# Kernel optimization log

Hardware: AMD Instinct MI355X
Metric: run time of the kernel (lower is better)

Reference implementation:

```python
import jax, jax.numpy as jnp
import numpy as np

N, M, E, H = 4096, 16384, 512, 8
D = E // H  # head dim = 64


def _rms(x, g, eps=1e-6):
    return x * jax.lax.rsqrt(jnp.mean(jnp.square(x), axis=-1, keepdims=True) + eps) * g


def _split(x):
    # (rows, E) -> (rows, H, D)
    return x.reshape(x.shape[0], H, D)


def _sdpa(q, k, v):
    # Faithful to the source layout: SDPA on (rows, H, D) tensors, i.e. per-row
    # attention over the H heads (tiny HxH softmax per node).
    s = jnp.einsum('nhd,ngd->nhg', q, k) / jnp.sqrt(jnp.asarray(D, q.dtype))
    a = jax.nn.softmax(s, axis=-1)
    return jnp.einsum('nhg,ngd->nhd', a, v).reshape(-1, E)


def setup_inputs() -> dict:
    key = jax.random.key(0)
    ks = jax.random.split(key, 25)
    w = lambda k, s, sc: jax.random.normal(k, s, dtype=jnp.float32) * sc
    se = 1.0 / np.sqrt(E)   # Linear(E, E) init scale
    sm = 1.0 / np.sqrt(M)   # Linear(M, N) init scale
    inp = {
        'x_node': jax.random.normal(ks[0], (N, E), dtype=jnp.float32),
        'x_edge': jax.random.normal(ks[1], (M, E), dtype=jnp.float32),
        # sparse-ish binary adjacency, avg degree ~8
        'adj': (jax.random.uniform(ks[2], (N, N)) < 0.002).astype(jnp.float32),
        # per-branch QKV weights (4 separate MultiHeadAttention modules)
        'Wq_hh': w(ks[3], (E, E), se), 'Wk_hh': w(ks[4], (E, E), se), 'Wv_hh': w(ks[5], (E, E), se),
        'Wq_ee': w(ks[6], (E, E), se), 'Wk_ee': w(ks[7], (E, E), se), 'Wv_ee': w(ks[8], (E, E), se),
        'Wq_he': w(ks[9], (E, E), se), 'Wk_he': w(ks[10], (E, E), se), 'Wv_he': w(ks[11], (E, E), se),
        'Wq_eh': w(ks[12], (E, E), se), 'Wk_eh': w(ks[13], (E, E), se), 'Wv_eh': w(ks[14], (E, E), se),
        # shape_proj (edges -> nodes) weights, one per module that uses it
        'Wp1_he': w(ks[15], (N, M), sm),
        'Wp1_eh': w(ks[16], (N, M), sm),
        'Wp1_ee': w(ks[17], (N, M), sm),
        # RMSNorm gains
        'g_n': jnp.ones((E,), jnp.float32),
        'g_e': jnp.ones((E,), jnp.float32),
        'g2': jnp.ones((E,), jnp.float32),
        # FeedForward
        'Wf1': w(ks[18], (E, 4 * E), se), 'bf1': jnp.zeros((4 * E,), jnp.float32),
        'Wf2': w(ks[19], (4 * E, E), 1.0 / np.sqrt(4 * E)), 'bf2': jnp.zeros((E,), jnp.float32),
    }
    return inp


def reference(x_node, x_edge, adj,
              Wq_hh, Wk_hh, Wv_hh, Wq_ee, Wk_ee, Wv_ee,
              Wq_he, Wk_he, Wv_he, Wq_eh, Wk_eh, Wv_eh,
              Wp1_he, Wp1_eh, Wp1_ee,
              g_n, g_e, g2, Wf1, bf1, Wf2, bf2):
    h = _rms(x_node, g_n)   # (N, E)
    e = _rms(x_edge, g_e)   # (M, E)

    # hh: adjacency injected into the node query branch
    q = jnp.einsum('nm,mhd->nhd', adj, _split(h @ Wq_hh))
    out_hh = _sdpa(q, _split(h @ Wk_hh), _split(h @ Wv_hh))

    # ee: edge queries/keys projected to node rows via shape_proj
    q = jnp.einsum('nm,mhd->nhd', Wp1_ee, _split(e @ Wq_ee))
    k = jnp.einsum('nm,mhd->nhd', Wp1_ee, _split(e @ Wk_ee))
    out_ee = _sdpa(q, k, _split(h @ Wv_ee))

    # eh: edge query projected to node rows, node key
    q = jnp.einsum('nm,mhd->nhd', Wp1_eh, _split(e @ Wq_eh))
    out_eh = _sdpa(q, _split(h @ Wk_eh), _split(h @ Wv_eh))

    # he: node query, edge key projected to node rows
    k = jnp.einsum('nm,mhd->nhd', Wp1_he, _split(e @ Wk_he))
    out_he = _sdpa(_split(h @ Wq_he), k, _split(h @ Wv_he))

    x = out_hh + out_ee + out_eh + out_he          # (N, E)
    y = _rms(x, g2)
    return jax.nn.gelu(y @ Wf1 + bf1, approximate=False) @ Wf2 + bf2
```

## Files before the change

### kernel.cpp

```cpp
#include <hip/hip_runtime.h>
#include <cstdint>


typedef unsigned short u16;
typedef __bf16 bf16x8 __attribute__((ext_vector_type(8)));
typedef float f32x4 __attribute__((ext_vector_type(4)));

__device__ __forceinline__ u16 f2bf(float f) {
    unsigned u = __float_as_uint(f);
    return (u16)((u + 0x7fffu + ((u >> 16) & 1u)) >> 16);
}
__device__ __forceinline__ float bf2f(u16 u) { return __uint_as_float(((unsigned)u) << 16); }
__device__ __forceinline__ float gelu_exact(float x) {
    return 0.5f * x * (1.0f + erff(x * 0.70710678118654752f));
}

__device__ __forceinline__ void gload_lds16(const void* g, void* l) {
    __builtin_amdgcn_global_load_lds(
        (const __attribute__((address_space(1))) unsigned int*)(uintptr_t)g,
        (__attribute__((address_space(3))) unsigned int*)(unsigned int)(uintptr_t)l,
        16, 0, 0);
}

__device__ __forceinline__ void swz_block(int& bx, int& by, int& bz) {
    const int nx = gridDim.x, ny = gridDim.y;
    const int nwg = nx * ny * gridDim.z;
    int lin = blockIdx.x + nx * (blockIdx.y + ny * blockIdx.z);
    const int chunk = nwg >> 3;
    lin = (lin & 7) * chunk + (lin >> 3);
    bx = lin % nx;
    lin /= nx;
    by = lin % ny;
    bz = lin / ny;
}

template <bool SWZ>
__global__ __launch_bounds__(256) void cvt_f32_bf16(const float* __restrict__ in,
                                                    u16* __restrict__ out, size_t n8) {
    size_t i = (size_t)blockIdx.x * 256 + threadIdx.x;
    size_t stride = (size_t)gridDim.x * 256;
    for (; i < n8; i += stride) {
        float4 a = ((const float4*)in)[i * 2];
        float4 b = ((const float4*)in)[i * 2 + 1];
        u16 r[8] = {f2bf(a.x), f2bf(a.y), f2bf(a.z), f2bf(a.w),
                    f2bf(b.x), f2bf(b.y), f2bf(b.z), f2bf(b.w)};
        size_t o = i;
        if constexpr (SWZ) o = (i & ~(size_t)63) | ((i & 63) ^ ((i >> 7) & 3));
        ((uint4*)out)[o] = *(const uint4*)r;
    }
}

__global__ __launch_bounds__(256) void transpose_cvt(const float* __restrict__ in,
                                                     u16* __restrict__ out, int R, int C) {
    __shared__ float tile[32][33];
    int c0 = blockIdx.x * 32, r0 = blockIdx.y * 32;
    int tx = threadIdx.x & 31, ty = threadIdx.x >> 5;
#pragma unroll
    for (int i = 0; i < 4; ++i)
        tile[ty + i * 8][tx] = in[(size_t)(r0 + ty + i * 8) * C + c0 + tx];
    __syncthreads();
#pragma unroll
    for (int i = 0; i < 4; ++i) {
        int orow = c0 + ty + i * 8;
        out[(size_t)orow * R + ((r0 + tx) ^ (((orow >> 1) & 3) << 3))] = f2bf(tile[tx][ty + i * 8]);
    }
}

struct W12 { const float* in[12]; u16* out[12]; };
__global__ __launch_bounds__(256) void transpose_cvt12(W12 w) {
    __shared__ float tile[32][33];
    const float* in = w.in[blockIdx.z];
    u16* out = w.out[blockIdx.z];
    int c0 = blockIdx.x * 32, r0 = blockIdx.y * 32;
    int tx = threadIdx.x & 31, ty = threadIdx.x >> 5;
#pragma unroll
    for (int i = 0; i < 4; ++i)
        tile[ty + i * 8][tx] = in[(size_t)(r0 + ty + i * 8) * 512 + c0 + tx];
    __syncthreads();
#pragma unroll
    for (int i = 0; i < 4; ++i) {
        int orow = c0 + ty + i * 8;
        out[(size_t)orow * 512 + ((r0 + tx) ^ (((orow >> 1) & 3) << 3))] = f2bf(tile[tx][ty + i * 8]);
    }
}

__global__ __launch_bounds__(256) void transpose_u16(const u16* __restrict__ in,
                                                     u16* __restrict__ out, int R, int C) {
    __shared__ u16 tile[32][34];
    int c0 = blockIdx.x * 32, r0 = blockIdx.y * 32;
    int tx = threadIdx.x & 31, ty = threadIdx.x >> 5;
#pragma unroll
    for (int i = 0; i < 4; ++i)
        tile[ty + i * 8][tx] = in[(size_t)(r0 + ty + i * 8) * C + c0 + tx];
    __syncthreads();
#pragma unroll
    for (int i = 0; i < 4; ++i) {
        int orow = c0 + ty + i * 8;
        out[(size_t)orow * R + ((r0 + tx) ^ (((orow >> 1) & 3) << 3))] = tile[tx][ty + i * 8];
    }
}

template <bool SWZ>
__global__ __launch_bounds__(256) void rmsnorm_bf16(const float* __restrict__ x,
                                                    const float* __restrict__ g,
                                                    u16* __restrict__ out) {
    int row = blockIdx.x, tid = threadIdx.x;
    const float* xr = x + (size_t)row * 512;
    float2 v = *(const float2*)(xr + tid * 2);
    float ss = v.x * v.x + v.y * v.y;
#pragma unroll
    for (int o = 32; o; o >>= 1) ss += __shfl_down(ss, o);
    __shared__ float red[4];
    if ((tid & 63) == 0) red[tid >> 6] = ss;
    __syncthreads();
    float tot = red[0] + red[1] + red[2] + red[3];
    float rs = rsqrtf(tot * (1.0f / 512.0f) + 1e-6f);
    unsigned pack = (unsigned)f2bf(v.x * rs * g[tid * 2]) |
                    ((unsigned)f2bf(v.y * rs * g[tid * 2 + 1]) << 16);
    int o32 = SWZ ? (tid ^ (((row >> 1) & 3) << 2)) : tid;
    ((unsigned*)out)[(size_t)row * 256 + o32] = pack;
}

__global__ __launch_bounds__(256) void adj_spmm(const float* __restrict__ adj,
                                                const u16* __restrict__ h,
                                                u16* __restrict__ out) {
    const int wave = threadIdx.x >> 6, lane = threadIdx.x & 63;
    const int n = blockIdx.x * 4 + wave;
    const float* arow = adj + (size_t)n * 4096;
    float acc[8] = {0.f, 0.f, 0.f, 0.f, 0.f, 0.f, 0.f, 0.f};
    for (int j = 0; j < 64; ++j) {
        float v = arow[j * 64 + lane];
        unsigned long long mask = __ballot(v != 0.0f);
        while (mask) {
            int bit = __ffsll((long long)mask) - 1;
            mask &= mask - 1;
            int m = j * 64 + bit;
            float w = __shfl(v, bit);
            int cs = (lane & ~3) | ((lane & 3) ^ ((m >> 1) & 3));
            uint4 q = *(const uint4*)(h + (size_t)m * 512 + cs * 8);
            const u16* qu = (const u16*)&q;
#pragma unroll
            for (int t = 0; t < 8; ++t) acc[t] += w * bf2f(qu[t]);
        }
    }
    int co = (lane & ~3) | ((lane & 3) ^ ((n >> 1) & 3));
    u16 r[8];
#pragma unroll
    for (int t = 0; t < 8; ++t) r[t] = f2bf(acc[t]);
    *(uint4*)(out + (size_t)n * 512 + co * 8) = *(const uint4*)r;
}

template <int MODE>
__device__ __forceinline__ void gemm_tile_body(const u16* __restrict__ A,
                                               const u16* __restrict__ Bt,
                                               int N, int K, int k_begin, int k_end,
                                               int rowStart, int colStart,
                                               void* __restrict__ C,
                                               const float* __restrict__ bias) {
    __shared__ u16 Asm[128 * 32];
    __shared__ u16 Bsm[128 * 32];
    const int tid = threadIdx.x;
    const int wave = tid >> 6, lane = tid & 63;
    const int wr = wave >> 1, wc = wave & 1;

    f32x4 acc[4][4];
#pragma unroll
    for (int m = 0; m < 4; ++m)
#pragma unroll
        for (int n = 0; n < 4; ++n) acc[m][n] = f32x4{0.f, 0.f, 0.f, 0.f};

    const int off0 = (wave * 2 + 0) * 1024 + lane * 16;
    const int off1 = (wave * 2 + 1) * 1024 + lane * 16;
    const int r0 = off0 >> 6, k0e = (off0 & 63) >> 1;
    const int r1 = off1 >> 6, k1e = (off1 & 63) >> 1;
    const size_t Arow0 = (size_t)(rowStart + r0) * K + k0e;
    const size_t Arow1 = (size_t)(rowStart + r1) * K + k1e;
    const size_t Brow0 = (size_t)(colStart + r0) * K + k0e;
    const size_t Brow1 = (size_t)(colStart + r1) * K + k1e;
    u16* As0 = &Asm[(wave * 2 + 0) * 512];
    u16* As1 = &Asm[(wave * 2 + 1) * 512];
    u16* Bs0 = &Bsm[(wave * 2 + 0) * 512];
    u16* Bs1 = &Bsm[(wave * 2 + 1) * 512];

    const int rsel = lane & 15, ksel = lane >> 4;
    const int fsw = (ksel ^ ((rsel >> 1) & 3)) << 3;

    for (int kk = k_begin; kk < k_end; kk += 32) {
        gload_lds16(A + Arow0 + kk, As0);
        gload_lds16(A + Arow1 + kk, As1);
        gload_lds16(Bt + Brow0 + kk, Bs0);
        gload_lds16(Bt + Brow1 + kk, Bs1);
        __syncthreads();
        bf16x8 aF[4], bF[4];
#pragma unroll
        for (int m = 0; m < 4; ++m)
            aF[m] = *(const bf16x8*)&Asm[(wr * 64 + m * 16 + rsel) * 32 + fsw];
#pragma unroll
        for (int n = 0; n < 4; ++n)
            bF[n] = *(const bf16x8*)&Bsm[(wc * 64 + n * 16 + rsel) * 32 + fsw];
#pragma unroll
        for (int m = 0; m < 4; ++m)
#pragma unroll
            for (int n = 0; n < 4; ++n)
                acc[m][n] = __builtin_amdgcn_mfma_f32_16x16x32_bf16(aF[m], bF[n], acc[m][n], 0, 0, 0);
        __syncthreads();
    }

    const int cq = (lane >> 4) * 4, cr = lane & 15;
#pragma unroll
    for (int m = 0; m < 4; ++m) {
#pragma unroll
        for (int n = 0; n < 4; ++n) {
            int col = colStart + wc * 64 + n * 16 + cr;
#pragma unroll
            for (int j = 0; j < 4; ++j) {
                int row = rowStart + wr * 64 + m * 16 + cq + j;
                float v = acc[m][n][j];
                if constexpr (MODE == 0) {
                    ((u16*)C)[(size_t)row * N + col] = f2bf(v);
                } else if constexpr (MODE == 1) {
                    v = gelu_exact(v + bias[col]);
                    ((u16*)C)[(size_t)row * N + (col ^ (((row >> 1) & 3) << 3))] = f2bf(v);
                } else {
                    if (bias) v += bias[col];
                    atomicAdd(&((float*)C)[(size_t)row * N + col], v);
                }
            }
        }
    }
}

template <int MODE>
__global__ __launch_bounds__(256) void gemm_bt(const u16* __restrict__ A,
                                               const u16* __restrict__ Bt,
                                               void* __restrict__ C,
                                               const float* __restrict__ bias,
                                               int N, int K, int kLen) {
    int bx, by, bz;
    swz_block(bx, by, bz);
    const float* bb = (MODE == 3) ? ((bz == 0) ? bias : nullptr) : bias;
    int kb = bz * kLen;
    gemm_tile_body<MODE>(A, Bt, N, K, kb, kb + kLen, by * 128, bx * 128, C, bb);
}

struct Small12 { const u16* A[12]; const u16* W[12]; u16* C[12]; };
__global__ __launch_bounds__(256) void gemm_small12(Small12 s) {
    int bx, by, bz;
    swz_block(bx, by, bz);
    gemm_tile_body<0>(s.A[bz], s.W[bz], 512, 512, 0, 512, by * 128, bx * 128, s.C[bz], nullptr);
}

struct Big3 { const float* A[3]; };
__global__ __launch_bounds__(256, 2) void gemm_f32a(Big3 ba, const u16* __restrict__ Bt,
                                                    float* __restrict__ C0, int K,
                                                    int zPerMat, int kLen) {
    __shared__ float Afs[128 * 32];
    __shared__ u16 Bsm[128 * 32];
    int bx, by, bz;
    swz_block(bx, by, bz);
    const int mat = bz / zPerMat, ks = bz - mat * zPerMat;
    const float* __restrict__ A = ba.A[mat];
    float* __restrict__ C = C0 + (size_t)mat * (4096 * 512);
    const int rowStart = by * 128, colStart = bx * 128;
    const int k0 = ks * kLen, kEnd = k0 + kLen;

    const int tid = threadIdx.x;
    const int wave = tid >> 6, lane = tid & 63;
    const int wr = wave >> 1, wc = wave & 1;

    f32x4 acc[4][4];
#pragma unroll
    for (int mm = 0; mm < 4; ++mm)
#pragma unroll
        for (int n = 0; n < 4; ++n) acc[mm][n] = f32x4{0.f, 0.f, 0.f, 0.f};

    const int lrow = lane >> 3;
    const int slot = (lane & 7) ^ lrow;
    size_t asrc[4];
    float* adst[4];
#pragma unroll
    for (int i = 0; i < 4; ++i) {
        int row = wave * 32 + i * 8 + lrow;
        asrc[i] = (size_t)(rowStart + row) * K + slot * 4;
        adst[i] = Afs + (wave * 4 + i) * 256 + lane * 4;
    }

    const int off0 = (wave * 2 + 0) * 1024 + lane * 16;
    const int off1 = (wave * 2 + 1) * 1024 + lane * 16;
    const int br0 = off0 >> 6, bk0 = (off0 & 63) >> 1;
    const int br1 = off1 >> 6, bk1 = (off1 & 63) >> 1;
    const u16* Bp0 = Bt + (size_t)(colStart + br0) * K + bk0;
    const u16* Bp1 = Bt + (size_t)(colStart + br1) * K + bk1;
    u16* Bs0 = &Bsm[(wave * 2 + 0) * 512];
    u16* Bs1 = &Bsm[(wave * 2 + 1) * 512];

    const int rsel = lane & 15, ksel = lane >> 4;
    const int fsw = (ksel ^ ((rsel >> 1) & 3)) << 3;

    for (int kk = k0; kk < kEnd; kk += 32) {
#pragma unroll
        for (int i = 0; i < 4; ++i)
            gload_lds16(A + asrc[i] + kk, adst[i]);
        gload_lds16(Bp0 + kk, Bs0);
        gload_lds16(Bp1 + kk, Bs1);
        __syncthreads();
        bf16x8 aF[4], bF[4];
#pragma unroll
        for (int mm = 0; mm < 4; ++mm) {
            int R = wr * 64 + mm * 16 + rsel;
            const char* rb = (const char*)Afs + R * 128;
            f32x4 lo = *(const f32x4*)(rb + ((((ksel << 1) | 0) ^ (R & 7)) << 4));
            f32x4 hi = *(const f32x4*)(rb + ((((ksel << 1) | 1) ^ (R & 7)) << 4));
            aF[mm][0] = (__bf16)lo[0]; aF[mm][1] = (__bf16)lo[1];
            aF[mm][2] = (__bf16)lo[2]; aF[mm][3] = (__bf16)lo[3];
            aF[mm][4] = (__bf16)hi[0]; aF[mm][5] = (__bf16)hi[1];
            aF[mm][6] = (__bf16)hi[2]; aF[mm][7] = (__bf16)hi[3];
        }
#pragma unroll
        for (int n = 0; n < 4; ++n)
            bF[n] = *(const bf16x8*)&Bsm[(wc * 64 + n * 16 + rsel) * 32 + fsw];
#pragma unroll
        for (int mm = 0; mm < 4; ++mm)
#pragma unroll
            for (int n = 0; n < 4; ++n)
                acc[mm][n] = __builtin_amdgcn_mfma_f32_16x16x32_bf16(aF[mm], bF[n], acc[mm][n], 0, 0, 0);
        __syncthreads();
    }

    const int cq = (lane >> 4) * 4, cr = lane & 15;
#pragma unroll
    for (int mm = 0; mm < 4; ++mm)
#pragma unroll
        for (int n = 0; n < 4; ++n) {
            int col = colStart + wc * 64 + n * 16 + cr;
#pragma unroll
            for (int j = 0; j < 4; ++j) {
                int row = rowStart + wr * 64 + mm * 16 + cq + j;
                atomicAdd(&C[(size_t)row * 512 + col], acc[mm][n][j]);
            }
        }
}

struct SP12 { const u16* p[12]; };
__global__ __launch_bounds__(256) void sdpa_fused(SP12 sp, const float* __restrict__ g2,
                                                  u16* __restrict__ y) {
    __shared__ float qb[4][8][65], kb[4][8][65], vb[4][8][65];
    __shared__ float aw[4][64];
    __shared__ float red[4];
    const int n = blockIdx.x, tid = threadIdx.x;
    const size_t base = (size_t)n * 512;
    const int e0 = tid * 2, hs = e0 >> 6, ds = e0 & 63;

#pragma unroll
    for (int br = 0; br < 4; ++br) {
        unsigned u;
        u = *(const unsigned*)(sp.p[br * 3 + 0] + base + e0);
        qb[br][hs][ds] = bf2f(u & 0xffffu); qb[br][hs][ds + 1] = bf2f(u >> 16);
        u = *(const unsigned*)(sp.p[br * 3 + 1] + base + e0);
        kb[br][hs][ds] = bf2f(u & 0xffffu); kb[br][hs][ds + 1] = bf2f(u >> 16);
        u = *(const unsigned*)(sp.p[br * 3 + 2] + base + e0);
        vb[br][hs][ds] = bf2f(u & 0xffffu); vb[br][hs][ds + 1] = bf2f(u >> 16);
    }
    __syncthreads();

    const int b = tid >> 6, h = (tid >> 3) & 7, g = tid & 7;
    float s = 0.f;
    const float* qr = &qb[b][h][0];
    const float* kr = &kb[b][g][0];
#pragma unroll
    for (int j = 0; j < 64; ++j) s += qr[j] * kr[j];
    s *= 0.125f;
    float mx = s;
#pragma unroll
    for (int o = 1; o < 8; o <<= 1) mx = fmaxf(mx, __shfl_xor(mx, o));
    float p = expf(s - mx);
    float sm = p;
#pragma unroll
    for (int o = 1; o < 8; o <<= 1) sm += __shfl_xor(sm, o);
    aw[b][(h << 3) | g] = p / sm;
    __syncthreads();

    float o0 = 0.f, o1 = 0.f;
#pragma unroll
    for (int bb = 0; bb < 4; ++bb)
#pragma unroll
        for (int gg = 0; gg < 8; ++gg) {
            float a = aw[bb][(hs << 3) | gg];
            o0 += a * vb[bb][gg][ds];
            o1 += a * vb[bb][gg][ds + 1];
        }

    float ss = o0 * o0 + o1 * o1;
#pragma unroll
    for (int o = 32; o; o >>= 1) ss += __shfl_down(ss, o);
    if ((tid & 63) == 0) red[tid >> 6] = ss;
    __syncthreads();
    float tot = red[0] + red[1] + red[2] + red[3];
    float rs = rsqrtf(tot * (1.0f / 512.0f) + 1e-6f);
    unsigned pack = (unsigned)f2bf(o0 * rs * g2[e0]) | ((unsigned)f2bf(o1 * rs * g2[e0 + 1]) << 16);
    ((unsigned*)y)[(size_t)n * 256 + (tid ^ (((n >> 1) & 3) << 2))] = pack;
}

extern "C" void kernel_launch(void* const* d_in, const int* in_sizes, int n_in,
                              void* d_out, int out_size, void* d_ws, size_t ws_size,
                              hipStream_t stream) {
    (void)in_sizes; (void)n_in; (void)out_size; (void)ws_size;
    const int N = 4096, M = 16384, E = 512;

    const float* x_node = (const float*)d_in[0];
    const float* x_edge = (const float*)d_in[1];
    const float* adj    = (const float*)d_in[2];
    const float* Wp1_he = (const float*)d_in[15];
    const float* Wp1_eh = (const float*)d_in[16];
    const float* Wp1_ee = (const float*)d_in[17];
    const float* g_n = (const float*)d_in[18];
    const float* g_e = (const float*)d_in[19];
    const float* g2  = (const float*)d_in[20];
    const float* Wf1 = (const float*)d_in[21];
    const float* bf1 = (const float*)d_in[22];
    const float* Wf2 = (const float*)d_in[23];
    const float* bf2 = (const float*)d_in[24];

    char* p = (char*)d_ws;
    auto alloc = [&](size_t b) { char* r = p; p += (b + 255) & ~(size_t)255; return r; };
    const size_t NP = (size_t)N * E;
    const size_t WSZ = (size_t)E * E;
    u16* h    = (u16*)alloc(NP * 2);
    u16* e    = (u16*)alloc((size_t)M * E * 2);
    u16* eT   = (u16*)alloc((size_t)M * E * 2);
    u16* Wt   = (u16*)alloc(12 * WSZ * 2);
    u16* Wf1T = (u16*)alloc((size_t)2048 * 512 * 2);
    u16* Wf2T = (u16*)alloc((size_t)512 * 2048 * 2);
    float* F3 = (float*)alloc(3 * NP * 4);
    u16* P3b  = (u16*)alloc(3 * NP * 2);
    u16* Ahb  = (u16*)alloc(NP * 2);
    u16* S12  = (u16*)alloc(12 * NP * 2);
    u16* y    = (u16*)alloc(NP * 2);
    u16* t    = (u16*)alloc((size_t)N * 2048 * 2);

    W12 w12;
    for (int i = 0; i < 12; ++i) { w12.in[i] = (const float*)d_in[3 + i]; w12.out[i] = Wt + i * WSZ; }
    transpose_cvt12<<<dim3(16, 16, 12), 256, 0, stream>>>(w12);
    transpose_cvt<<<dim3(64, 16), 256, 0, stream>>>(Wf1, Wf1T, 512, 2048);
    transpose_cvt<<<dim3(16, 64), 256, 0, stream>>>(Wf2, Wf2T, 2048, 512);

    rmsnorm_bf16<true><<<N, 256, 0, stream>>>(x_node, g_n, h);
    rmsnorm_bf16<false><<<M, 256, 0, stream>>>(x_edge, g_e, e);
    transpose_u16<<<dim3(16, 512), 256, 0, stream>>>(e, eT, M, 512);
    adj_spmm<<<1024, 256, 0, stream>>>(adj, h, Ahb);

    hipMemsetAsync(F3, 0, 3 * NP * 4, stream);
    Big3 bp; bp.A[0] = Wp1_ee; bp.A[1] = Wp1_eh; bp.A[2] = Wp1_he;
    gemm_f32a<<<dim3(4, 32, 12), 256, 0, stream>>>(bp, eT, F3, M, 4, 4096);
    cvt_f32_bf16<true><<<2048, 256, 0, stream>>>(F3, P3b, 3 * NP / 8);
    const u16* Peeb = P3b + 0 * NP;
    const u16* Pehb = P3b + 1 * NP;
    const u16* Pheb = P3b + 2 * NP;

    Small12 sb;
    const u16* aList[12] = {Ahb, h, h, Peeb, Peeb, h, Pehb, h, h, h, Pheb, h};
    const int wList[12]  = {0, 1, 2, 3, 4, 5, 9, 10, 11, 6, 7, 8};
    for (int i = 0; i < 12; ++i) {
        sb.A[i] = aList[i];
        sb.W[i] = Wt + wList[i] * WSZ;
        sb.C[i] = S12 + i * NP;
    }
    gemm_small12<<<dim3(4, 32, 12), 256, 0, stream>>>(sb);

    SP12 sp;
    for (int i = 0; i < 12; ++i) sp.p[i] = S12 + i * NP;
    sdpa_fused<<<N, 256, 0, stream>>>(sp, g2, y);

    gemm_bt<1><<<dim3(16, 32, 1), 256, 0, stream>>>(y, Wf1T, t, bf1, 2048, 512, 512);
    hipMemsetAsync(d_out, 0, NP * 4, stream);
    gemm_bt<3><<<dim3(4, 32, 2), 256, 0, stream>>>(t, Wf2T, d_out, bf2, 512, 2048, 1024);
}
```

Baseline: 638.2 us.

## Double-buffer LDS tiles in GEMM kernels to overlap loads with MFMA

Both the bf16 GEMM body and the fp32-A GEMM now use two LDS buffers, issuing the global-to-LDS load for the next K tile before computing on the current one. Only one barrier per K step remains. The goal is to hide global load latency behind MFMA work. It doubles shared memory per block, and the launch_bounds min-blocks hint of 2 is dropped from gemm_f32a, so occupancy may fall.

New measurement: 706.9 us. 1.11x slower.

```diff
diff --git a/kernel.cpp b/kernel.cpp
--- a/kernel.cpp
+++ b/kernel.cpp
@@ -157,8 +157,8 @@
                                                int rowStart, int colStart,
                                                void* __restrict__ C,
                                                const float* __restrict__ bias) {
-    __shared__ u16 Asm[128 * 32];
-    __shared__ u16 Bsm[128 * 32];
+    __shared__ u16 Asm[2][4096];
+    __shared__ u16 Bsm[2][4096];
     const int tid = threadIdx.x;
     const int wave = tid >> 6, lane = tid & 63;
     const int wr = wave >> 1, wc = wave & 1;
@@ -177,33 +177,44 @@
     const size_t Arow1 = (size_t)(rowStart + r1) * K + k1e;
     const size_t Brow0 = (size_t)(colStart + r0) * K + k0e;
     const size_t Brow1 = (size_t)(colStart + r1) * K + k1e;
-    u16* As0 = &Asm[(wave * 2 + 0) * 512];
-    u16* As1 = &Asm[(wave * 2 + 1) * 512];
-    u16* Bs0 = &Bsm[(wave * 2 + 0) * 512];
-    u16* Bs1 = &Bsm[(wave * 2 + 1) * 512];
+    const int ws0 = (wave * 2 + 0) * 512, ws1 = (wave * 2 + 1) * 512;
 
     const int rsel = lane & 15, ksel = lane >> 4;
     const int fsw = (ksel ^ ((rsel >> 1) & 3)) << 3;
 
-    for (int kk = k_begin; kk < k_end; kk += 32) {
-        gload_lds16(A + Arow0 + kk, As0);
-        gload_lds16(A + Arow1 + kk, As1);
-        gload_lds16(Bt + Brow0 + kk, Bs0);
-        gload_lds16(Bt + Brow1 + kk, Bs1);
-        __syncthreads();
+    auto STAGE = [&](int buf, int kk) {
+        gload_lds16(A + Arow0 + kk, &Asm[buf][ws0]);
+        gload_lds16(A + Arow1 + kk, &Asm[buf][ws1]);
+        gload_lds16(Bt + Brow0 + kk, &Bsm[buf][ws0]);
+        gload_lds16(Bt + Brow1 + kk, &Bsm[buf][ws1]);
+    };
+    auto COMPUTE = [&](int buf) {
         bf16x8 aF[4], bF[4];
 #pragma unroll
         for (int m = 0; m < 4; ++m)
-            aF[m] = *(const bf16x8*)&Asm[(wr * 64 + m * 16 + rsel) * 32 + fsw];
+            aF[m] = *(const bf16x8*)&Asm[buf][(wr * 64 + m * 16 + rsel) * 32 + fsw];
 #pragma unroll
         for (int n = 0; n < 4; ++n)
-            bF[n] = *(const bf16x8*)&Bsm[(wc * 64 + n * 16 + rsel) * 32 + fsw];
+            bF[n] = *(const bf16x8*)&Bsm[buf][(wc * 64 + n * 16 + rsel) * 32 + fsw];
 #pragma unroll
         for (int m = 0; m < 4; ++m)
 #pragma unroll
             for (int n = 0; n < 4; ++n)
                 acc[m][n] = __builtin_amdgcn_mfma_f32_16x16x32_bf16(aF[m], bF[n], acc[m][n], 0, 0, 0);
+    };
+
+    const int nt = (k_end - k_begin) >> 5;
+    STAGE(0, k_begin);
+    __syncthreads();
+    for (int t = 0; t < nt; t += 2) {
+        if (t + 1 < nt) STAGE(1, k_begin + (t + 1) * 32);
+        COMPUTE(0);
         __syncthreads();
+        if (t + 1 < nt) {
+            if (t + 2 < nt) STAGE(0, k_begin + (t + 2) * 32);
+            COMPUTE(1);
+            __syncthreads();
+        }
     }
 
     const int cq = (lane >> 4) * 4, cr = lane & 15;
@@ -251,18 +262,18 @@
 }
 
 struct Big3 { const float* A[3]; };
-__global__ __launch_bounds__(256, 2) void gemm_f32a(Big3 ba, const u16* __restrict__ Bt,
-                                                    float* __restrict__ C0, int K,
-                                                    int zPerMat, int kLen) {
-    __shared__ float Afs[128 * 32];
-    __shared__ u16 Bsm[128 * 32];
+__global__ __launch_bounds__(256) void gemm_f32a(Big3 ba, const u16* __restrict__ Bt,
+                                                 float* __restrict__ C0, int K,
+                                                 int zPerMat, int kLen) {
+    __shared__ float Afs[2][4096];
+    __shared__ u16 Bsm[2][4096];
     int bx, by, bz;
     swz_block(bx, by, bz);
     const int mat = bz / zPerMat, ks = bz - mat * zPerMat;
     const float* __restrict__ A = ba.A[mat];
     float* __restrict__ C = C0 + (size_t)mat * (4096 * 512);
     const int rowStart = by * 128, colStart = bx * 128;
-    const int k0 = ks * kLen, kEnd = k0 + kLen;
+    const int k0 = ks * kLen;
 
     const int tid = threadIdx.x;
     const int wave = tid >> 6, lane = tid & 63;
@@ -277,12 +288,12 @@
     const int lrow = lane >> 3;
     const int slot = (lane & 7) ^ lrow;
     size_t asrc[4];
-    float* adst[4];
+    int adst[4];
 #pragma unroll
     for (int i = 0; i < 4; ++i) {
         int row = wave * 32 + i * 8 + lrow;
         asrc[i] = (size_t)(rowStart + row) * K + slot * 4;
-        adst[i] = Afs + (wave * 4 + i) * 256 + lane * 4;
+        adst[i] = (wave * 4 + i) * 256 + lane * 4;
     }
 
     const int off0 = (wave * 2 + 0) * 1024 + lane * 16;
@@ -291,24 +302,24 @@
     const int br1 = off1 >> 6, bk1 = (off1 & 63) >> 1;
     const u16* Bp0 = Bt + (size_t)(colStart + br0) * K + bk0;
     const u16* Bp1 = Bt + (size_t)(colStart + br1) * K + bk1;
-    u16* Bs0 = &Bsm[(wave * 2 + 0) * 512];
-    u16* Bs1 = &Bsm[(wave * 2 + 1) * 512];
+    const int ws0 = (wave * 2 + 0) * 512, ws1 = (wave * 2 + 1) * 512;
 
     const int rsel = lane & 15, ksel = lane >> 4;
     const int fsw = (ksel ^ ((rsel >> 1) & 3)) << 3;
 
-    for (int kk = k0; kk < kEnd; kk += 32) {
+    auto STAGE = [&](int buf, int kk) {
 #pragma unroll
         for (int i = 0; i < 4; ++i)
-            gload_lds16(A + asrc[i] + kk, adst[i]);
-        gload_lds16(Bp0 + kk, Bs0);
-        gload_lds16(Bp1 + kk, Bs1);
-        __syncthreads();
+            gload_lds16(A + asrc[i] + kk, &Afs[buf][adst[i]]);
+        gload_lds16(Bp0 + kk, &Bsm[buf][ws0]);
+        gload_lds16(Bp1 + kk, &Bsm[buf][ws1]);
+    };
+    auto COMPUTE = [&](int buf) {
         bf16x8 aF[4], bF[4];
 #pragma unroll
         for (int mm = 0; mm < 4; ++mm) {
             int R = wr * 64 + mm * 16 + rsel;
-            const char* rb = (const char*)Afs + R * 128;
+            const char* rb = (const char*)&Afs[buf][0] + R * 128;
             f32x4 lo = *(const f32x4*)(rb + ((((ksel << 1) | 0) ^ (R & 7)) << 4));
             f32x4 hi = *(const f32x4*)(rb + ((((ksel << 1) | 1) ^ (R & 7)) << 4));
             aF[mm][0] = (__bf16)lo[0]; aF[mm][1] = (__bf16)lo[1];
@@ -318,13 +329,26 @@
         }
 #pragma unroll
         for (int n = 0; n < 4; ++n)
-            bF[n] = *(const bf16x8*)&Bsm[(wc * 64 + n * 16 + rsel) * 32 + fsw];
+            bF[n] = *(const bf16x8*)&Bsm[buf][(wc * 64 + n * 16 + rsel) * 32 + fsw];
 #pragma unroll
         for (int mm = 0; mm < 4; ++mm)
 #pragma unroll
             for (int n = 0; n < 4; ++n)
                 acc[mm][n] = __builtin_amdgcn_mfma_f32_16x16x32_bf16(aF[mm], bF[n], acc[mm][n], 0, 0, 0);
+    };
+
+    const int nt = kLen >> 5;
+    STAGE(0, k0);
+    __syncthreads();
+    for (int t = 0; t < nt; t += 2) {
+        if (t + 1 < nt) STAGE(1, k0 + (t + 1) * 32);
+        COMPUTE(0);
         __syncthreads();
+        if (t + 1 < nt) {
+            if (t + 2 < nt) STAGE(0, k0 + (t + 2) * 32);
+            COMPUTE(1);
+            __syncthreads();
+        }
     }
 
     const int cq = (lane >> 4) * 4, cr = lane & 15;
```

## Double-buffer LDS tiles in f32-A GEMM to overlap loads with MFMA

Applied to the files above, without the earlier changes.

Turns the single-buffered shared-memory K loop of gemm_f32a into a two-stage ping-pong pipeline. The next k-tile is fetched with global_load_lds into the alternate buffer while MFMAs run on the current one, and a partial vmcnt wait allows exactly one stage of loads in flight. This is meant to hide global memory latency that used to be fully exposed before each compute step. LDS use doubles to about 48KB per block, which may cut occupancy below the 2 blocks per CU the launch bounds ask for.

After: 624.0 us. -2.2%, faster.

```diff
diff --git a/kernel.cpp b/kernel.cpp
--- a/kernel.cpp
+++ b/kernel.cpp
@@ -254,15 +254,15 @@
 __global__ __launch_bounds__(256, 2) void gemm_f32a(Big3 ba, const u16* __restrict__ Bt,
                                                     float* __restrict__ C0, int K,
                                                     int zPerMat, int kLen) {
-    __shared__ float Afs[128 * 32];
-    __shared__ u16 Bsm[128 * 32];
+    __shared__ float Afs[2][4096];
+    __shared__ u16 Bsm[2][4096];
     int bx, by, bz;
     swz_block(bx, by, bz);
     const int mat = bz / zPerMat, ks = bz - mat * zPerMat;
     const float* __restrict__ A = ba.A[mat];
     float* __restrict__ C = C0 + (size_t)mat * (4096 * 512);
     const int rowStart = by * 128, colStart = bx * 128;
-    const int k0 = ks * kLen, kEnd = k0 + kLen;
+    const int k0 = ks * kLen;
 
     const int tid = threadIdx.x;
     const int wave = tid >> 6, lane = tid & 63;
@@ -277,12 +277,12 @@
     const int lrow = lane >> 3;
     const int slot = (lane & 7) ^ lrow;
     size_t asrc[4];
-    float* adst[4];
+    int adst[4];
 #pragma unroll
     for (int i = 0; i < 4; ++i) {
         int row = wave * 32 + i * 8 + lrow;
         asrc[i] = (size_t)(rowStart + row) * K + slot * 4;
-        adst[i] = Afs + (wave * 4 + i) * 256 + lane * 4;
+        adst[i] = (wave * 4 + i) * 256 + lane * 4;
     }
 
     const int off0 = (wave * 2 + 0) * 1024 + lane * 16;
@@ -291,24 +291,24 @@
     const int br1 = off1 >> 6, bk1 = (off1 & 63) >> 1;
     const u16* Bp0 = Bt + (size_t)(colStart + br0) * K + bk0;
     const u16* Bp1 = Bt + (size_t)(colStart + br1) * K + bk1;
-    u16* Bs0 = &Bsm[(wave * 2 + 0) * 512];
-    u16* Bs1 = &Bsm[(wave * 2 + 1) * 512];
+    const int ws0 = (wave * 2 + 0) * 512, ws1 = (wave * 2 + 1) * 512;
 
     const int rsel = lane & 15, ksel = lane >> 4;
     const int fsw = (ksel ^ ((rsel >> 1) & 3)) << 3;
 
-    for (int kk = k0; kk < kEnd; kk += 32) {
+    auto STAGE = [&](int buf, int kk) {
 #pragma unroll
         for (int i = 0; i < 4; ++i)
-            gload_lds16(A + asrc[i] + kk, adst[i]);
-        gload_lds16(Bp0 + kk, Bs0);
-        gload_lds16(Bp1 + kk, Bs1);
-        __syncthreads();
+            gload_lds16(A + asrc[i] + kk, &Afs[buf][adst[i]]);
+        gload_lds16(Bp0 + kk, &Bsm[buf][ws0]);
+        gload_lds16(Bp1 + kk, &Bsm[buf][ws1]);
+    };
+    auto COMPUTE = [&](int buf) {
         bf16x8 aF[4], bF[4];
 #pragma unroll
         for (int mm = 0; mm < 4; ++mm) {
             int R = wr * 64 + mm * 16 + rsel;
-            const char* rb = (const char*)Afs + R * 128;
+            const char* rb = (const char*)&Afs[buf][0] + R * 128;
             f32x4 lo = *(const f32x4*)(rb + ((((ksel << 1) | 0) ^ (R & 7)) << 4));
             f32x4 hi = *(const f32x4*)(rb + ((((ksel << 1) | 1) ^ (R & 7)) << 4));
             aF[mm][0] = (__bf16)lo[0]; aF[mm][1] = (__bf16)lo[1];
@@ -318,14 +318,40 @@
         }
 #pragma unroll
         for (int n = 0; n < 4; ++n)
-            bF[n] = *(const bf16x8*)&Bsm[(wc * 64 + n * 16 + rsel) * 32 + fsw];
+            bF[n] = *(const bf16x8*)&Bsm[buf][(wc * 64 + n * 16 + rsel) * 32 + fsw];
 #pragma unroll
         for (int mm = 0; mm < 4; ++mm)
 #pragma unroll
             for (int n = 0; n < 4; ++n)
                 acc[mm][n] = __builtin_amdgcn_mfma_f32_16x16x32_bf16(aF[mm], bF[n], acc[mm][n], 0, 0, 0);
-        __syncthreads();
-    }
+    };
+
+    const int nt = kLen >> 5;
+    STAGE(0, k0);
+    asm volatile("s_waitcnt vmcnt(0)");
+    __builtin_amdgcn_sched_barrier(0);
+    __builtin_amdgcn_s_barrier();
+    __builtin_amdgcn_sched_barrier(0);
+
+    int cur = 0;
+    for (int t = 0; t < nt - 1; ++t) {
+        STAGE(cur ^ 1, k0 + (t + 1) * 32);
+        __builtin_amdgcn_sched_barrier(0);
+        asm volatile("s_waitcnt vmcnt(6)");
+        __builtin_amdgcn_sched_barrier(0);
+        __builtin_amdgcn_s_barrier();
+        __builtin_amdgcn_sched_barrier(0);
+        COMPUTE(cur);
+        __builtin_amdgcn_sched_barrier(0);
+        __builtin_amdgcn_s_barrier();
+        __builtin_amdgcn_sched_barrier(0);
+        cur ^= 1;
+    }
+    asm volatile("s_waitcnt vmcnt(0)");
+    __builtin_amdgcn_sched_barrier(0);
+    __builtin_amdgcn_s_barrier();
+    __builtin_amdgcn_sched_barrier(0);
+    COMPUTE(cur);
 
     const int cq = (lane >> 4) * 4, cr = lane & 15;
 #pragma unroll
```
